# Optimization experiments

Measured on AMD Instinct MI355X. Metric: run time of the kernel, lower is better.

## Reference

```python
import jax, jax.numpy as jnp
import numpy as np

ITERATIONS = 100  # resonator iterations (default in __init__)


def _quantize(x):
    # MAP/bipolar quantize: sign with ties -> +1
    return jnp.where(x >= 0, 1.0, -1.0).astype(x.dtype)


def _resonator_step(inp, estimates, codebooks):
    # inp: (b, d); estimates: (b, f, d); codebooks: (f, v, d)
    f = estimates.shape[-2]
    # rolled copies, stacked: (b, f, f-1, d); product = multibind of all other factors
    rolled = jnp.stack([jnp.roll(estimates, i, axis=-3 + 1) for i in range(1, f)], axis=-2)
    inv_others = jnp.prod(rolled, axis=-2)              # (b, f, d)
    new_estimates = inp[:, None, :] * inv_others        # bind, (b, f, d)
    similarity = jnp.einsum('bfd,fvd->bfv', new_estimates, codebooks)  # (b, f, v)
    # multiset with similarity weights, then quantize
    output = _quantize(jnp.einsum('bfv,fvd->bfd', similarity, codebooks))
    max_sim = jnp.max(similarity, axis=-1)              # (b, f)
    return output, max_sim


def setup_inputs() -> dict:
    key = jax.random.key(0)
    b, f, v, d = 1024, 4, 64, 2048
    k1, k2 = jax.random.split(key)
    # bipolar codebooks (f, v, d)
    codebooks = _quantize(jax.random.normal(k1, (f, v, d), dtype=jnp.float32))
    # construct a solvable input: bind of one random codevector per factor
    idx = jax.random.randint(k2, (b, f), 0, v)          # (b, f)
    chosen = codebooks[jnp.arange(f)[None, :], idx]     # (b, f, d)
    inp = jnp.prod(chosen, axis=1)                      # (b, d)
    # init estimates: quantized multiset (bundle) of each codebook, tiled over batch
    init = _quantize(jnp.sum(codebooks, axis=1))        # (f, d)
    init_estimates = jnp.broadcast_to(init[None], (b, f, d)).astype(jnp.float32)
    return {"input": inp, "init_estimates": init_estimates, "codebooks": codebooks}


def reference(input, init_estimates, codebooks):
    # Concurrent resonator network, fixed iteration count (data-dependent
    # early-convergence check omitted for jit compatibility).
    def body(est, _):
        out, max_sim = _resonator_step(input, est, codebooks)
        return out, max_sim

    estimates, max_sims = jax.lax.scan(body, init_estimates, None, length=ITERATIONS)
    # cleanup: argmax of |similarity| against codebooks (argmax_abs=True)
    sim = jnp.einsum('bfd,fvd->bfv', estimates, codebooks)
    outcome = jnp.argmax(jnp.abs(sim), axis=-1).astype(jnp.int32)  # (b, f)
    convergence = jnp.int32(ITERATIONS - 1)
    return estimates, outcome, max_sims[-1], convergence
```

## Files before the change

### kernel.cpp

```cpp
#include <hip/hip_runtime.h>
#include <stdint.h>


#define NB 1024
#define NF 4
#define ND 2048
#define NW 32
#define ITERS 100

#define OFF_OUT  (NB*NF*ND)
#define OFF_MS   (OFF_OUT + NB*NF)
#define OFF_CONV (OFF_MS + NB*NF)

typedef unsigned long long u64;

__global__ void pack_cb_kernel(const float* __restrict__ cb,
                               u64* __restrict__ cbB, u64* __restrict__ cbT) {
    const int lane = threadIdx.x & 63;
    const int gw   = (blockIdx.x * (blockDim.x >> 6)) + (threadIdx.x >> 6);
    const int nw   = (gridDim.x * blockDim.x) >> 6;
    for (int idx = gw; idx < NF * 64 * NW; idx += nw) {
        const int j = idx >> 11, v = (idx >> 5) & 63, w = idx & 31;
        const float x = cb[(((j << 6) | v) << 11) + (w << 6) + lane];
        const u64 m = __ballot(x < 0.0f);
        if (lane == 0) cbB[(((j << 5) | w) << 6) | v] = m;
    }
    for (int idx = gw; idx < NF * ND; idx += nw) {
        const int j = idx >> 11, d = idx & 2047;
        const float x = cb[(((j << 6) | lane) << 11) + d];
        const u64 m = __ballot(x < 0.0f);
        if (lane == 0) cbT[idx] = m;
    }
}

__global__ __launch_bounds__(256, 2) void resonator_kernel(
    const float* __restrict__ inp, const float* __restrict__ est_init,
    const u64* __restrict__ cbB, const u64* __restrict__ cbT,
    float* __restrict__ out) {
    __shared__ u64 s_hist[4][NF][NW];
    __shared__ u64 s_inp[NW];
    __shared__ u64 s_ne[NF][NW];
    __shared__ int s_conv[NF];

    const int b    = blockIdx.x;
    const int tid  = threadIdx.x;
    const int j    = tid >> 6;
    const int lane = tid & 63;

    const u64* cbBj = cbB + (j << 11);
    const u64* cbTj = cbT + (j << 11);

    #pragma unroll
    for (int k = 0; k < 8; ++k) {
        const int w = (j << 3) + k;
        const u64 m = __ballot(inp[(b << 11) + (w << 6) + lane] < 0.0f);
        if (lane == 0) s_inp[w] = m;
    }
    #pragma unroll 4
    for (int w = 0; w < NW; ++w) {
        const u64 m = __ballot(
            est_init[(((b << 2) | j) << 11) + (w << 6) + lane] < 0.0f);
        if (lane == 0) s_hist[0][j][w] = m;
    }
    __syncthreads();

    int m_last = 0, m_prev = 0, final_slot = 0;

    for (int it = 0; it < ITERS; ++it) {
        const int cur = it & 3, nxt = (it + 1) & 3, prv = (it + 3) & 3;

        if (lane < NW) {
            const u64 X = s_inp[lane]
                        ^ s_hist[cur][0][lane] ^ s_hist[cur][1][lane]
                        ^ s_hist[cur][2][lane] ^ s_hist[cur][3][lane];
            s_ne[j][lane] = X ^ s_hist[cur][j][lane];
        }

        int pc = 0;
        #pragma unroll
        for (int ch = 0; ch < 4; ++ch) {
            const int w8 = ch << 3;
            const u64 g0 = cbBj[((w8 + 0) << 6) | lane];
            const u64 g1 = cbBj[((w8 + 1) << 6) | lane];
            const u64 g2 = cbBj[((w8 + 2) << 6) | lane];
            const u64 g3 = cbBj[((w8 + 3) << 6) | lane];
            const u64 g4 = cbBj[((w8 + 4) << 6) | lane];
            const u64 g5 = cbBj[((w8 + 5) << 6) | lane];
            const u64 g6 = cbBj[((w8 + 6) << 6) | lane];
            const u64 g7 = cbBj[((w8 + 7) << 6) | lane];
            pc += (int)__popcll(s_ne[j][w8 + 0] ^ g0)
                + (int)__popcll(s_ne[j][w8 + 1] ^ g1)
                + (int)__popcll(s_ne[j][w8 + 2] ^ g2)
                + (int)__popcll(s_ne[j][w8 + 3] ^ g3)
                + (int)__popcll(s_ne[j][w8 + 4] ^ g4)
                + (int)__popcll(s_ne[j][w8 + 5] ^ g5)
                + (int)__popcll(s_ne[j][w8 + 6] ^ g6)
                + (int)__popcll(s_ne[j][w8 + 7] ^ g7);
        }

        int mn = pc, spc = pc;
        #pragma unroll
        for (int off = 32; off > 0; off >>= 1) {
            const int a1 = __shfl_xor(mn, off);
            const int a2 = __shfl_xor(spc, off);
            mn = mn < a1 ? mn : a1;
            spc += a2;
        }
        m_prev = m_last;
        m_last = ND - 2 * mn;

        const int mean = spc >> 6;
        const int dev  = pc - mean;
        const int devc = dev < -128 ? -128 : (dev > 127 ? 127 : dev);
        const int ex   = dev - devc;
        const int u    = devc + 128;
        const u64 c0 = __ballot(u & 1),  c1 = __ballot(u & 2);
        const u64 c2 = __ballot(u & 4),  c3 = __ballot(u & 8);
        const u64 c4 = __ballot(u & 16), c5 = __ballot(u & 32);
        const u64 c6 = __ballot(u & 64), c7 = __ballot(u & 128);
        u64 om = __ballot(ex != 0);
        const int nout = (int)__popcll(om);
        int ov0 = 0, ov1 = 0, oe0 = 0, oe1 = 0;
        if (nout > 0) {
            ov0 = __builtin_ctzll(om); om &= om - 1;
            oe0 = 4 * __builtin_amdgcn_readlane(ex, ov0);
            if (nout > 1) {
                ov1 = __builtin_ctzll(om); om &= om - 1;
                oe1 = 4 * __builtin_amdgcn_readlane(ex, ov1);
            }
        }
        const int base = 131072 - 2 * spc;
        const int cmul = 4 * mean - 4608;

        #pragma unroll
        for (int ch = 0; ch < 8; ++ch) {
            const int w4 = ch << 2;
            const u64 ga = cbTj[((w4 + 0) << 6) | lane];
            const u64 gb = cbTj[((w4 + 1) << 6) | lane];
            const u64 gc = cbTj[((w4 + 2) << 6) | lane];
            const u64 gd = cbTj[((w4 + 3) << 6) | lane];
            #pragma unroll
            for (int k2 = 0; k2 < 4; ++k2) {
                const u64 cw = (k2 == 0) ? ga : (k2 == 1) ? gb
                             : (k2 == 2) ? gc : gd;
                int t = base + cmul * (int)__popcll(cw);
                t += (int)__popcll(c0 & cw) << 2;
                t += (int)__popcll(c1 & cw) << 3;
                t += (int)__popcll(c2 & cw) << 4;
                t += (int)__popcll(c3 & cw) << 5;
                t += (int)__popcll(c4 & cw) << 6;
                t += (int)__popcll(c5 & cw) << 7;
                t += (int)__popcll(c6 & cw) << 8;
                t += (int)__popcll(c7 & cw) << 9;
                t += oe0 * (int)((cw >> ov0) & 1);
                t += oe1 * (int)((cw >> ov1) & 1);
                if (nout > 2) {
                    u64 m2 = om;
                    while (m2) {
                        const int vv = __builtin_ctzll(m2); m2 &= m2 - 1;
                        const int ee = 4 * __builtin_amdgcn_readlane(ex, vv);
                        t += ee * (int)((cw >> vv) & 1);
                    }
                }
                const u64 nww = __ballot(t < 0);
                if (lane == 0) s_hist[nxt][j][w4 + k2] = nww;
            }
        }

        int df1 = 0, df2 = 0;
        if (lane < NW) {
            const u64 a = s_hist[nxt][j][lane];
            df1 = (a != s_hist[cur][j][lane]);
            df2 = (a != s_hist[prv][j][lane]);
        }
        const u64 b1 = __ballot(df1), b2 = __ballot(df2);
        if (lane == 0) s_conv[j] = (b1 == 0 ? 1 : 0) | (b2 == 0 ? 2 : 0);
        __syncthreads();

        const int fl = s_conv[0] & s_conv[1] & s_conv[2] & s_conv[3];
        final_slot = nxt;
        if (fl & 1) break;
        if (it >= 1 && (fl & 2)) {
            if (((ITERS - it) & 1) == 0) { final_slot = cur; m_last = m_prev; }
            break;
        }
    }

    int pcO = 0;
    #pragma unroll
    for (int w = 0; w < NW; ++w)
        pcO += (int)__popcll(s_hist[final_slot][j][w] ^ cbBj[(w << 6) | lane]);
    const int simF = ND - (pcO << 1);
    const int aF   = simF < 0 ? -simF : simF;
    int key = (aF << 6) | (63 - lane);
    #pragma unroll
    for (int off = 32; off > 0; off >>= 1) {
        const int t1 = __shfl_xor(key, off);
        key = key > t1 ? key : t1;
    }
    if (lane == 0) {
        out[OFF_OUT + (b << 2) + j] = (float)(63 - (key & 63));
        out[OFF_MS  + (b << 2) + j] = (float)m_last;
    }

    #pragma unroll 4
    for (int k = 0; k < 32; ++k) {
        const int idx = tid + (k << 8);
        const int jj = idx >> 11, d = idx & 2047;
        const u64 wrd = s_hist[final_slot][jj][d >> 6];
        out[(b << 13) + idx] = ((wrd >> (d & 63)) & 1) ? -1.0f : 1.0f;
    }
    if (b == 0 && tid == 0) out[OFF_CONV] = 99.0f;
}

extern "C" void kernel_launch(void* const* d_in, const int* in_sizes, int n_in,
                              void* d_out, int out_size, void* d_ws, size_t ws_size,
                              hipStream_t stream) {
    const float* inp  = (const float*)d_in[0];
    const float* est0 = (const float*)d_in[1];
    const float* cb   = (const float*)d_in[2];
    float* out = (float*)d_out;
    u64* cbB = (u64*)d_ws;
    u64* cbT = cbB + NF * 64 * NW;

    pack_cb_kernel<<<64, 256, 0, stream>>>(cb, cbB, cbT);
    resonator_kernel<<<NB, 256, 0, stream>>>(inp, est0, cbB, cbT, out);
}
```

Before: 1.743 ms.

## Process two batch rows per block to share codebook loads

Each block now runs the resonator iterations for two batch rows at once, so every codebook word loaded from global memory (cbB and cbT) and its column popcount is used for both rows. The grid is halved to NB/2 blocks. This cuts codebook traffic and load latency per row and gives more independent work per wave to hide latency. In exchange it raises register pressure, which may reduce occupancy. The early exit now waits until both rows have converged, so some rows may run extra iterations.

```diff
diff --git a/kernel.cpp b/kernel.cpp
--- a/kernel.cpp
+++ b/kernel.cpp
@@ -37,100 +37,123 @@
     const float* __restrict__ inp, const float* __restrict__ est_init,
     const u64* __restrict__ cbB, const u64* __restrict__ cbT,
     float* __restrict__ out) {
-    __shared__ u64 s_hist[4][NF][NW];
-    __shared__ u64 s_inp[NW];
-    __shared__ u64 s_ne[NF][NW];
-    __shared__ int s_conv[NF];
+    __shared__ u64 s_hist[2][4][NF][NW];
+    __shared__ u64 s_inp[2][NW];
+    __shared__ u64 s_ne[2][NF][NW];
+    __shared__ int s_conv[2][NF];
 
     const int b    = blockIdx.x;
     const int tid  = threadIdx.x;
     const int j    = tid >> 6;
     const int lane = tid & 63;
+    const int rA   = b << 1;
 
     const u64* cbBj = cbB + (j << 11);
     const u64* cbTj = cbT + (j << 11);
 
     #pragma unroll
-    for (int k = 0; k < 8; ++k) {
-        const int w = (j << 3) + k;
-        const u64 m = __ballot(inp[(b << 11) + (w << 6) + lane] < 0.0f);
-        if (lane == 0) s_inp[w] = m;
-    }
-    #pragma unroll 4
-    for (int w = 0; w < NW; ++w) {
-        const u64 m = __ballot(
-            est_init[(((b << 2) | j) << 11) + (w << 6) + lane] < 0.0f);
-        if (lane == 0) s_hist[0][j][w] = m;
+    for (int r = 0; r < 2; ++r) {
+        #pragma unroll
+        for (int k = 0; k < 8; ++k) {
+            const int w = (j << 3) + k;
+            const u64 m = __ballot(inp[((rA + r) << 11) + (w << 6) + lane] < 0.0f);
+            if (lane == 0) s_inp[r][w] = m;
+        }
+        #pragma unroll 4
+        for (int w = 0; w < NW; ++w) {
+            const u64 m = __ballot(
+                est_init[((((rA + r) << 2) | j) << 11) + (w << 6) + lane] < 0.0f);
+            if (lane == 0) s_hist[r][0][j][w] = m;
+        }
     }
     __syncthreads();
 
-    int m_last = 0, m_prev = 0, final_slot = 0;
+    int mlA = 0, mpA = 0, fsA = 0;
+    int mlB = 0, mpB = 0, fsB = 0;
 
     for (int it = 0; it < ITERS; ++it) {
         const int cur = it & 3, nxt = (it + 1) & 3, prv = (it + 3) & 3;
 
         if (lane < NW) {
-            const u64 X = s_inp[lane]
-                        ^ s_hist[cur][0][lane] ^ s_hist[cur][1][lane]
-                        ^ s_hist[cur][2][lane] ^ s_hist[cur][3][lane];
-            s_ne[j][lane] = X ^ s_hist[cur][j][lane];
-        }
-
-        int pc = 0;
-        #pragma unroll
-        for (int ch = 0; ch < 4; ++ch) {
-            const int w8 = ch << 3;
-            const u64 g0 = cbBj[((w8 + 0) << 6) | lane];
-            const u64 g1 = cbBj[((w8 + 1) << 6) | lane];
-            const u64 g2 = cbBj[((w8 + 2) << 6) | lane];
-            const u64 g3 = cbBj[((w8 + 3) << 6) | lane];
-            const u64 g4 = cbBj[((w8 + 4) << 6) | lane];
-            const u64 g5 = cbBj[((w8 + 5) << 6) | lane];
-            const u64 g6 = cbBj[((w8 + 6) << 6) | lane];
-            const u64 g7 = cbBj[((w8 + 7) << 6) | lane];
-            pc += (int)__popcll(s_ne[j][w8 + 0] ^ g0)
-                + (int)__popcll(s_ne[j][w8 + 1] ^ g1)
-                + (int)__popcll(s_ne[j][w8 + 2] ^ g2)
-                + (int)__popcll(s_ne[j][w8 + 3] ^ g3)
-                + (int)__popcll(s_ne[j][w8 + 4] ^ g4)
-                + (int)__popcll(s_ne[j][w8 + 5] ^ g5)
-                + (int)__popcll(s_ne[j][w8 + 6] ^ g6)
-                + (int)__popcll(s_ne[j][w8 + 7] ^ g7);
-        }
-
-        int mn = pc, spc = pc;
+            const u64 XA = s_inp[0][lane]
+                ^ s_hist[0][cur][0][lane] ^ s_hist[0][cur][1][lane]
+                ^ s_hist[0][cur][2][lane] ^ s_hist[0][cur][3][lane];
+            s_ne[0][j][lane] = XA ^ s_hist[0][cur][j][lane];
+            const u64 XB = s_inp[1][lane]
+                ^ s_hist[1][cur][0][lane] ^ s_hist[1][cur][1][lane]
+                ^ s_hist[1][cur][2][lane] ^ s_hist[1][cur][3][lane];
+            s_ne[1][j][lane] = XB ^ s_hist[1][cur][j][lane];
+        }
+
+        int pcA = 0, pcB = 0;
+        #pragma unroll
+        for (int ch = 0; ch < 8; ++ch) {
+            const int w4 = ch << 2;
+            const u64 g0 = cbBj[((w4 + 0) << 6) | lane];
+            const u64 g1 = cbBj[((w4 + 1) << 6) | lane];
+            const u64 g2 = cbBj[((w4 + 2) << 6) | lane];
+            const u64 g3 = cbBj[((w4 + 3) << 6) | lane];
+            pcA += (int)__popcll(s_ne[0][j][w4 + 0] ^ g0)
+                 + (int)__popcll(s_ne[0][j][w4 + 1] ^ g1)
+                 + (int)__popcll(s_ne[0][j][w4 + 2] ^ g2)
+                 + (int)__popcll(s_ne[0][j][w4 + 3] ^ g3);
+            pcB += (int)__popcll(s_ne[1][j][w4 + 0] ^ g0)
+                 + (int)__popcll(s_ne[1][j][w4 + 1] ^ g1)
+                 + (int)__popcll(s_ne[1][j][w4 + 2] ^ g2)
+                 + (int)__popcll(s_ne[1][j][w4 + 3] ^ g3);
+        }
+
+        int mnA = pcA, spA = pcA, mnB = pcB, spB = pcB;
         #pragma unroll
         for (int off = 32; off > 0; off >>= 1) {
-            const int a1 = __shfl_xor(mn, off);
-            const int a2 = __shfl_xor(spc, off);
-            mn = mn < a1 ? mn : a1;
-            spc += a2;
-        }
-        m_prev = m_last;
-        m_last = ND - 2 * mn;
-
-        const int mean = spc >> 6;
-        const int dev  = pc - mean;
-        const int devc = dev < -128 ? -128 : (dev > 127 ? 127 : dev);
-        const int ex   = dev - devc;
-        const int u    = devc + 128;
-        const u64 c0 = __ballot(u & 1),  c1 = __ballot(u & 2);
-        const u64 c2 = __ballot(u & 4),  c3 = __ballot(u & 8);
-        const u64 c4 = __ballot(u & 16), c5 = __ballot(u & 32);
-        const u64 c6 = __ballot(u & 64), c7 = __ballot(u & 128);
-        u64 om = __ballot(ex != 0);
-        const int nout = (int)__popcll(om);
-        int ov0 = 0, ov1 = 0, oe0 = 0, oe1 = 0;
-        if (nout > 0) {
-            ov0 = __builtin_ctzll(om); om &= om - 1;
-            oe0 = 4 * __builtin_amdgcn_readlane(ex, ov0);
-            if (nout > 1) {
-                ov1 = __builtin_ctzll(om); om &= om - 1;
-                oe1 = 4 * __builtin_amdgcn_readlane(ex, ov1);
+            const int a1 = __shfl_xor(mnA, off), a2 = __shfl_xor(spA, off);
+            const int a3 = __shfl_xor(mnB, off), a4 = __shfl_xor(spB, off);
+            mnA = mnA < a1 ? mnA : a1;  spA += a2;
+            mnB = mnB < a3 ? mnB : a3;  spB += a4;
+        }
+        mpA = mlA; mlA = ND - 2 * mnA;
+        mpB = mlB; mlB = ND - 2 * mnB;
+
+        const int meanA = spA >> 6, devA = pcA - meanA;
+        const int devcA = devA < -128 ? -128 : (devA > 127 ? 127 : devA);
+        const int exA = devA - devcA, uA = devcA + 128;
+        const int meanB = spB >> 6, devB = pcB - meanB;
+        const int devcB = devB < -128 ? -128 : (devB > 127 ? 127 : devB);
+        const int exB = devB - devcB, uB = devcB + 128;
+
+        const u64 cA0 = __ballot(uA & 1),  cA1 = __ballot(uA & 2);
+        const u64 cA2 = __ballot(uA & 4),  cA3 = __ballot(uA & 8);
+        const u64 cA4 = __ballot(uA & 16), cA5 = __ballot(uA & 32);
+        const u64 cA6 = __ballot(uA & 64), cA7 = __ballot(uA & 128);
+        const u64 cB0 = __ballot(uB & 1),  cB1 = __ballot(uB & 2);
+        const u64 cB2 = __ballot(uB & 4),  cB3 = __ballot(uB & 8);
+        const u64 cB4 = __ballot(uB & 16), cB5 = __ballot(uB & 32);
+        const u64 cB6 = __ballot(uB & 64), cB7 = __ballot(uB & 128);
+
+        u64 omA = __ballot(exA != 0);
+        const int novA = (int)__popcll(omA);
+        int ovA0 = 0, ovA1 = 0, oeA0 = 0, oeA1 = 0;
+        if (novA > 0) {
+            ovA0 = __builtin_ctzll(omA); omA &= omA - 1;
+            oeA0 = 4 * __builtin_amdgcn_readlane(exA, ovA0);
+            if (novA > 1) {
+                ovA1 = __builtin_ctzll(omA); omA &= omA - 1;
+                oeA1 = 4 * __builtin_amdgcn_readlane(exA, ovA1);
             }
         }
-        const int base = 131072 - 2 * spc;
-        const int cmul = 4 * mean - 4608;
+        u64 omB = __ballot(exB != 0);
+        const int novB = (int)__popcll(omB);
+        int ovB0 = 0, ovB1 = 0, oeB0 = 0, oeB1 = 0;
+        if (novB > 0) {
+            ovB0 = __builtin_ctzll(omB); omB &= omB - 1;
+            oeB0 = 4 * __builtin_amdgcn_readlane(exB, ovB0);
+            if (novB > 1) {
+                ovB1 = __builtin_ctzll(omB); omB &= omB - 1;
+                oeB1 = 4 * __builtin_amdgcn_readlane(exB, ovB1);
+            }
+        }
+        const int baseA = 131072 - 2 * spA, cmulA = 4 * meanA - 4608;
+        const int baseB = 131072 - 2 * spB, cmulB = 4 * meanB - 4608;
 
         #pragma unroll
         for (int ch = 0; ch < 8; ++ch) {
@@ -143,72 +166,110 @@
             for (int k2 = 0; k2 < 4; ++k2) {
                 const u64 cw = (k2 == 0) ? ga : (k2 == 1) ? gb
                              : (k2 == 2) ? gc : gd;
-                int t = base + cmul * (int)__popcll(cw);
-                t += (int)__popcll(c0 & cw) << 2;
-                t += (int)__popcll(c1 & cw) << 3;
-                t += (int)__popcll(c2 & cw) << 4;
-                t += (int)__popcll(c3 & cw) << 5;
-                t += (int)__popcll(c4 & cw) << 6;
-                t += (int)__popcll(c5 & cw) << 7;
-                t += (int)__popcll(c6 & cw) << 8;
-                t += (int)__popcll(c7 & cw) << 9;
-                t += oe0 * (int)((cw >> ov0) & 1);
-                t += oe1 * (int)((cw >> ov1) & 1);
-                if (nout > 2) {
-                    u64 m2 = om;
+                const int colb = (int)__popcll(cw);
+                int tA = baseA + cmulA * colb;
+                tA += (int)__popcll(cA0 & cw) << 2;
+                tA += (int)__popcll(cA1 & cw) << 3;
+                tA += (int)__popcll(cA2 & cw) << 4;
+                tA += (int)__popcll(cA3 & cw) << 5;
+                tA += (int)__popcll(cA4 & cw) << 6;
+                tA += (int)__popcll(cA5 & cw) << 7;
+                tA += (int)__popcll(cA6 & cw) << 8;
+                tA += (int)__popcll(cA7 & cw) << 9;
+                tA += oeA0 * (int)((cw >> ovA0) & 1);
+                tA += oeA1 * (int)((cw >> ovA1) & 1);
+                if (novA > 2) {
+                    u64 m2 = omA;
                     while (m2) {
                         const int vv = __builtin_ctzll(m2); m2 &= m2 - 1;
-                        const int ee = 4 * __builtin_amdgcn_readlane(ex, vv);
-                        t += ee * (int)((cw >> vv) & 1);
+                        tA += 4 * __builtin_amdgcn_readlane(exA, vv)
+                                * (int)((cw >> vv) & 1);
                     }
                 }
-                const u64 nww = __ballot(t < 0);
-                if (lane == 0) s_hist[nxt][j][w4 + k2] = nww;
+                int tB = baseB + cmulB * colb;
+                tB += (int)__popcll(cB0 & cw) << 2;
+                tB += (int)__popcll(cB1 & cw) << 3;
+                tB += (int)__popcll(cB2 & cw) << 4;
+                tB += (int)__popcll(cB3 & cw) << 5;
+                tB += (int)__popcll(cB4 & cw) << 6;
+                tB += (int)__popcll(cB5 & cw) << 7;
+                tB += (int)__popcll(cB6 & cw) << 8;
+                tB += (int)__popcll(cB7 & cw) << 9;
+                tB += oeB0 * (int)((cw >> ovB0) & 1);
+                tB += oeB1 * (int)((cw >> ovB1) & 1);
+                if (novB > 2) {
+                    u64 m2 = omB;
+                    while (m2) {
+                        const int vv = __builtin_ctzll(m2); m2 &= m2 - 1;
+                        tB += 4 * __builtin_amdgcn_readlane(exB, vv)
+                                * (int)((cw >> vv) & 1);
+                    }
+                }
+                const u64 nwA = __ballot(tA < 0);
+                const u64 nwB = __ballot(tB < 0);
+                if (lane == 0) {
+                    s_hist[0][nxt][j][w4 + k2] = nwA;
+                    s_hist[1][nxt][j][w4 + k2] = nwB;
+                }
             }
         }
 
-        int df1 = 0, df2 = 0;
+        int d1A = 0, d2A = 0, d1B = 0, d2B = 0;
         if (lane < NW) {
-            const u64 a = s_hist[nxt][j][lane];
-            df1 = (a != s_hist[cur][j][lane]);
-            df2 = (a != s_hist[prv][j][lane]);
-        }
-        const u64 b1 = __ballot(df1), b2 = __ballot(df2);
-        if (lane == 0) s_conv[j] = (b1 == 0 ? 1 : 0) | (b2 == 0 ? 2 : 0);
+            const u64 aA = s_hist[0][nxt][j][lane];
+            d1A = (aA != s_hist[0][cur][j][lane]);
+            d2A = (aA != s_hist[0][prv][j][lane]);
+            const u64 aB = s_hist[1][nxt][j][lane];
+            d1B = (aB != s_hist[1][cur][j][lane]);
+            d2B = (aB != s_hist[1][prv][j][lane]);
+        }
+        const u64 bA1 = __ballot(d1A), bA2 = __ballot(d2A);
+        const u64 bB1 = __ballot(d1B), bB2 = __ballot(d2B);
+        if (lane == 0) {
+            s_conv[0][j] = (bA1 == 0 ? 1 : 0) | (bA2 == 0 ? 2 : 0);
+            s_conv[1][j] = (bB1 == 0 ? 1 : 0) | (bB2 == 0 ? 2 : 0);
+        }
         __syncthreads();
 
-        const int fl = s_conv[0] & s_conv[1] & s_conv[2] & s_conv[3];
-        final_slot = nxt;
-        if (fl & 1) break;
-        if (it >= 1 && (fl & 2)) {
-            if (((ITERS - it) & 1) == 0) { final_slot = cur; m_last = m_prev; }
+        const int flA = s_conv[0][0] & s_conv[0][1] & s_conv[0][2] & s_conv[0][3];
+        const int flB = s_conv[1][0] & s_conv[1][1] & s_conv[1][2] & s_conv[1][3];
+        fsA = nxt; fsB = nxt;
+        const bool okA = (flA & 1) || (it >= 1 && (flA & 2));
+        const bool okB = (flB & 1) || (it >= 1 && (flB & 2));
+        if (okA && okB) {
+            if (!(flA & 1) && ((ITERS - it) & 1) == 0) { fsA = cur; mlA = mpA; }
+            if (!(flB & 1) && ((ITERS - it) & 1) == 0) { fsB = cur; mlB = mpB; }
             break;
         }
     }
 
-    int pcO = 0;
     #pragma unroll
-    for (int w = 0; w < NW; ++w)
-        pcO += (int)__popcll(s_hist[final_slot][j][w] ^ cbBj[(w << 6) | lane]);
-    const int simF = ND - (pcO << 1);
-    const int aF   = simF < 0 ? -simF : simF;
-    int key = (aF << 6) | (63 - lane);
-    #pragma unroll
-    for (int off = 32; off > 0; off >>= 1) {
-        const int t1 = __shfl_xor(key, off);
-        key = key > t1 ? key : t1;
-    }
-    if (lane == 0) {
-        out[OFF_OUT + (b << 2) + j] = (float)(63 - (key & 63));
-        out[OFF_MS  + (b << 2) + j] = (float)m_last;
-    }
-
-    #pragma unroll 4
-    for (int k = 0; k < 32; ++k) {
-        const int idx = tid + (k << 8);
-        const int jj = idx >> 11, d = idx & 2047;
-        const u64 wrd = s_hist[final_slot][jj][d >> 6];
-        out[(b << 13) + idx] = ((wrd >> (d & 63)) & 1) ? -1.0f : 1.0f;
+    for (int r = 0; r < 2; ++r) {
+        const int fs = r ? fsB : fsA;
+        const int ml = r ? mlB : mlA;
+        int pcO = 0;
+        #pragma unroll
+        for (int w = 0; w < NW; ++w)
+            pcO += (int)__popcll(s_hist[r][fs][j][w] ^ cbBj[(w << 6) | lane]);
+        const int simF = ND - (pcO << 1);
+        const int aF   = simF < 0 ? -simF : simF;
+        int key = (aF << 6) | (63 - lane);
+        #pragma unroll
+        for (int off = 32; off > 0; off >>= 1) {
+            const int t1 = __shfl_xor(key, off);
+            key = key > t1 ? key : t1;
+        }
+        if (lane == 0) {
+            out[OFF_OUT + ((rA + r) << 2) + j] = (float)(63 - (key & 63));
+            out[OFF_MS  + ((rA + r) << 2) + j] = (float)ml;
+        }
+        #pragma unroll 4
+        for (int k = 0; k < 32; ++k) {
+            const int idx = tid + (k << 8);
+            const int jj = idx >> 11, d = idx & 2047;
+            const u64 wrd = s_hist[r][fs][jj][d >> 6];
+            out[((rA + r) << 13) + idx] = ((wrd >> (d & 63)) & 1) ? -1.0f : 1.0f;
+        }
     }
     if (b == 0 && tid == 0) out[OFF_CONV] = 99.0f;
 }
@@ -224,5 +285,5 @@
     u64* cbT = cbB + NF * 64 * NW;
 
     pack_cb_kernel<<<64, 256, 0, stream>>>(cb, cbB, cbT);
-    resonator_kernel<<<NB, 256, 0, stream>>>(inp, est0, cbB, cbT, out);
+    resonator_kernel<<<NB / 2, 256, 0, stream>>>(inp, est0, cbB, cbT, out);
 }
```

New measurement: 1.730 ms. No clear change (-0.7%).

## Stage packed codebooks in LDS and process four batch rows per block

Applied to the files above, without the earlier changes.

Each block now handles four batch rows with 1024 threads and copies the bit-packed codebooks (both orientations) into shared memory once. The per-iteration similarity and multiset loops read them as 128-bit pairs from LDS instead of 64-bit global loads, and the pack layout is interleaved to support this. The history ring shrinks to three slots with rotating indices. Early exit now requires all four rows in a block to have converged, so rows that settle early may run extra iterations. The grid also shrinks to 256 blocks, which reduces parallelism.

```diff
diff --git a/kernel.cpp b/kernel.cpp
--- a/kernel.cpp
+++ b/kernel.cpp
@@ -7,6 +7,7 @@
 #define ND 2048
 #define NW 32
 #define ITERS 100
+#define NRB 4
 
 #define OFF_OUT  (NB*NF*ND)
 #define OFF_MS   (OFF_OUT + NB*NF)
@@ -23,93 +24,115 @@
         const int j = idx >> 11, v = (idx >> 5) & 63, w = idx & 31;
         const float x = cb[(((j << 6) | v) << 11) + (w << 6) + lane];
         const u64 m = __ballot(x < 0.0f);
-        if (lane == 0) cbB[(((j << 5) | w) << 6) | v] = m;
+        if (lane == 0)
+            cbB[(((((j << 4) | (w >> 1)) << 6) | v) << 1) | (w & 1)] = m;
     }
     for (int idx = gw; idx < NF * ND; idx += nw) {
         const int j = idx >> 11, d = idx & 2047;
         const float x = cb[(((j << 6) | lane) << 11) + d];
         const u64 m = __ballot(x < 0.0f);
-        if (lane == 0) cbT[idx] = m;
+        const int w = d >> 6, la = d & 63;
+        if (lane == 0)
+            cbT[(((((j << 4) | (w >> 1)) << 6) | la) << 1) | (w & 1)] = m;
     }
 }
 
-__global__ __launch_bounds__(256, 2) void resonator_kernel(
+#define PCW(CW, W)                                                           \
+    {                                                                        \
+        const u64 cw_ = (CW);                                                \
+        int t = base + cmul * (int)__popcll(cw_);                            \
+        t += (int)__popcll(c0 & cw_) << 2;                                   \
+        t += (int)__popcll(c1 & cw_) << 3;                                   \
+        t += (int)__popcll(c2 & cw_) << 4;                                   \
+        t += (int)__popcll(c3 & cw_) << 5;                                   \
+        t += (int)__popcll(c4 & cw_) << 6;                                   \
+        t += (int)__popcll(c5 & cw_) << 7;                                   \
+        t += (int)__popcll(c6 & cw_) << 8;                                   \
+        t += (int)__popcll(c7 & cw_) << 9;                                   \
+        t += oe0 * (int)((cw_ >> ov0) & 1);                                  \
+        t += oe1 * (int)((cw_ >> ov1) & 1);                                  \
+        if (nov > 2) {                              \
+            u64 m2 = om;                                                     \
+            while (m2) {                                                     \
+                const int vv = __builtin_ctzll(m2); m2 &= m2 - 1;            \
+                t += 4 * __builtin_amdgcn_readlane(ex, vv)                   \
+                       * (int)((cw_ >> vv) & 1);                             \
+            }                                                                \
+        }                                                                    \
+        const u64 nww = __ballot(t < 0);                                     \
+        if (lane == 0) s_hist[r][nxt][j][W] = nww;                           \
+    }
+
+__global__ __launch_bounds__(1024, 4) void resonator_kernel(
     const float* __restrict__ inp, const float* __restrict__ est_init,
     const u64* __restrict__ cbB, const u64* __restrict__ cbT,
     float* __restrict__ out) {
-    __shared__ u64 s_hist[4][NF][NW];
-    __shared__ u64 s_inp[NW];
-    __shared__ u64 s_ne[NF][NW];
-    __shared__ int s_conv[NF];
+    __shared__ u64 l_cbB[NF * 16 * 64 * 2];
+    __shared__ u64 l_cbT[NF * 16 * 64 * 2];
+    __shared__ u64 s_hist[NRB][3][NF][NW];
+    __shared__ u64 s_inp[NRB][NW];
+    __shared__ u64 s_ne[NRB][NF][NW];
+    __shared__ int s_conv[NRB][NF];
+    __shared__ int s_fs[NRB];
 
     const int b    = blockIdx.x;
     const int tid  = threadIdx.x;
-    const int j    = tid >> 6;
+    const int wid  = tid >> 6;
     const int lane = tid & 63;
-
-    const u64* cbBj = cbB + (j << 11);
-    const u64* cbTj = cbT + (j << 11);
-
+    const int j    = wid & 3;
+    const int r    = wid >> 2;
+    const int row  = (b << 2) + r;
+
+    for (int idx = tid; idx < NF * 16 * 64 * 2; idx += 1024) {
+        l_cbB[idx] = cbB[idx];
+        l_cbT[idx] = cbT[idx];
+    }
     #pragma unroll
     for (int k = 0; k < 8; ++k) {
         const int w = (j << 3) + k;
-        const u64 m = __ballot(inp[(b << 11) + (w << 6) + lane] < 0.0f);
-        if (lane == 0) s_inp[w] = m;
+        const u64 m = __ballot(inp[(row << 11) + (w << 6) + lane] < 0.0f);
+        if (lane == 0) s_inp[r][w] = m;
     }
     #pragma unroll 4
     for (int w = 0; w < NW; ++w) {
         const u64 m = __ballot(
-            est_init[(((b << 2) | j) << 11) + (w << 6) + lane] < 0.0f);
-        if (lane == 0) s_hist[0][j][w] = m;
+            est_init[(((row << 2) | j) << 11) + (w << 6) + lane] < 0.0f);
+        if (lane == 0) s_hist[r][0][j][w] = m;
     }
     __syncthreads();
 
-    int m_last = 0, m_prev = 0, final_slot = 0;
+    const ulonglong2* tB = (const ulonglong2*)l_cbB + (j << 10) + lane;
+    const ulonglong2* tT = (const ulonglong2*)l_cbT + (j << 10) + lane;
+
+    int ml = 0, mp = 0, fs = 0;
+    int cur = 0, nxt = 1, prv = 2;
 
     for (int it = 0; it < ITERS; ++it) {
-        const int cur = it & 3, nxt = (it + 1) & 3, prv = (it + 3) & 3;
-
         if (lane < NW) {
-            const u64 X = s_inp[lane]
-                        ^ s_hist[cur][0][lane] ^ s_hist[cur][1][lane]
-                        ^ s_hist[cur][2][lane] ^ s_hist[cur][3][lane];
-            s_ne[j][lane] = X ^ s_hist[cur][j][lane];
+            const u64 X = s_inp[r][lane]
+                ^ s_hist[r][cur][0][lane] ^ s_hist[r][cur][1][lane]
+                ^ s_hist[r][cur][2][lane] ^ s_hist[r][cur][3][lane];
+            s_ne[r][j][lane] = X ^ s_hist[r][cur][j][lane];
         }
 
         int pc = 0;
         #pragma unroll
-        for (int ch = 0; ch < 4; ++ch) {
-            const int w8 = ch << 3;
-            const u64 g0 = cbBj[((w8 + 0) << 6) | lane];
-            const u64 g1 = cbBj[((w8 + 1) << 6) | lane];
-            const u64 g2 = cbBj[((w8 + 2) << 6) | lane];
-            const u64 g3 = cbBj[((w8 + 3) << 6) | lane];
-            const u64 g4 = cbBj[((w8 + 4) << 6) | lane];
-            const u64 g5 = cbBj[((w8 + 5) << 6) | lane];
-            const u64 g6 = cbBj[((w8 + 6) << 6) | lane];
-            const u64 g7 = cbBj[((w8 + 7) << 6) | lane];
-            pc += (int)__popcll(s_ne[j][w8 + 0] ^ g0)
-                + (int)__popcll(s_ne[j][w8 + 1] ^ g1)
-                + (int)__popcll(s_ne[j][w8 + 2] ^ g2)
-                + (int)__popcll(s_ne[j][w8 + 3] ^ g3)
-                + (int)__popcll(s_ne[j][w8 + 4] ^ g4)
-                + (int)__popcll(s_ne[j][w8 + 5] ^ g5)
-                + (int)__popcll(s_ne[j][w8 + 6] ^ g6)
-                + (int)__popcll(s_ne[j][w8 + 7] ^ g7);
-        }
-
-        int mn = pc, spc = pc;
+        for (int w2 = 0; w2 < 16; ++w2) {
+            const ulonglong2 g  = tB[w2 << 6];
+            const ulonglong2 nn = *(const ulonglong2*)&s_ne[r][j][w2 << 1];
+            pc += (int)__popcll(nn.x ^ g.x) + (int)__popcll(nn.y ^ g.y);
+        }
+        int mn = pc, sp = pc;
         #pragma unroll
         for (int off = 32; off > 0; off >>= 1) {
             const int a1 = __shfl_xor(mn, off);
-            const int a2 = __shfl_xor(spc, off);
+            const int a2 = __shfl_xor(sp, off);
             mn = mn < a1 ? mn : a1;
-            spc += a2;
-        }
-        m_prev = m_last;
-        m_last = ND - 2 * mn;
-
-        const int mean = spc >> 6;
+            sp += a2;
+        }
+        mp = ml; ml = ND - 2 * mn;
+
+        const int mean = sp >> 6;
         const int dev  = pc - mean;
         const int devc = dev < -128 ? -128 : (dev > 127 ? 127 : dev);
         const int ex   = dev - devc;
@@ -119,77 +142,62 @@
         const u64 c4 = __ballot(u & 16), c5 = __ballot(u & 32);
         const u64 c6 = __ballot(u & 64), c7 = __ballot(u & 128);
         u64 om = __ballot(ex != 0);
-        const int nout = (int)__popcll(om);
+        const int nov = (int)__popcll(om);
         int ov0 = 0, ov1 = 0, oe0 = 0, oe1 = 0;
-        if (nout > 0) {
+        if (nov > 0) {
             ov0 = __builtin_ctzll(om); om &= om - 1;
             oe0 = 4 * __builtin_amdgcn_readlane(ex, ov0);
-            if (nout > 1) {
+            if (nov > 1) {
                 ov1 = __builtin_ctzll(om); om &= om - 1;
                 oe1 = 4 * __builtin_amdgcn_readlane(ex, ov1);
             }
         }
-        const int base = 131072 - 2 * spc;
+        const int base = 131072 - 2 * sp;
         const int cmul = 4 * mean - 4608;
 
         #pragma unroll
-        for (int ch = 0; ch < 8; ++ch) {
-            const int w4 = ch << 2;
-            const u64 ga = cbTj[((w4 + 0) << 6) | lane];
-            const u64 gb = cbTj[((w4 + 1) << 6) | lane];
-            const u64 gc = cbTj[((w4 + 2) << 6) | lane];
-            const u64 gd = cbTj[((w4 + 3) << 6) | lane];
-            #pragma unroll
-            for (int k2 = 0; k2 < 4; ++k2) {
-                const u64 cw = (k2 == 0) ? ga : (k2 == 1) ? gb
-                             : (k2 == 2) ? gc : gd;
-                int t = base + cmul * (int)__popcll(cw);
-                t += (int)__popcll(c0 & cw) << 2;
-                t += (int)__popcll(c1 & cw) << 3;
-                t += (int)__popcll(c2 & cw) << 4;
-                t += (int)__popcll(c3 & cw) << 5;
-                t += (int)__popcll(c4 & cw) << 6;
-                t += (int)__popcll(c5 & cw) << 7;
-                t += (int)__popcll(c6 & cw) << 8;
-                t += (int)__popcll(c7 & cw) << 9;
-                t += oe0 * (int)((cw >> ov0) & 1);
-                t += oe1 * (int)((cw >> ov1) & 1);
-                if (nout > 2) {
-                    u64 m2 = om;
-                    while (m2) {
-                        const int vv = __builtin_ctzll(m2); m2 &= m2 - 1;
-                        const int ee = 4 * __builtin_amdgcn_readlane(ex, vv);
-                        t += ee * (int)((cw >> vv) & 1);
-                    }
-                }
-                const u64 nww = __ballot(t < 0);
-                if (lane == 0) s_hist[nxt][j][w4 + k2] = nww;
-            }
-        }
-
-        int df1 = 0, df2 = 0;
+        for (int w2 = 0; w2 < 16; ++w2) {
+            const ulonglong2 g = tT[w2 << 6];
+            PCW(g.x, (w2 << 1))
+            PCW(g.y, (w2 << 1) + 1)
+        }
+
+        int d1 = 0, d2 = 0;
         if (lane < NW) {
-            const u64 a = s_hist[nxt][j][lane];
-            df1 = (a != s_hist[cur][j][lane]);
-            df2 = (a != s_hist[prv][j][lane]);
-        }
-        const u64 b1 = __ballot(df1), b2 = __ballot(df2);
-        if (lane == 0) s_conv[j] = (b1 == 0 ? 1 : 0) | (b2 == 0 ? 2 : 0);
+            const u64 a = s_hist[r][nxt][j][lane];
+            d1 = (a != s_hist[r][cur][j][lane]);
+            d2 = (a != s_hist[r][prv][j][lane]);
+        }
+        const u64 b1 = __ballot(d1), b2 = __ballot(d2);
+        if (lane == 0) s_conv[r][j] = (b1 == 0 ? 1 : 0) | (b2 == 0 ? 2 : 0);
         __syncthreads();
 
-        const int fl = s_conv[0] & s_conv[1] & s_conv[2] & s_conv[3];
-        final_slot = nxt;
-        if (fl & 1) break;
-        if (it >= 1 && (fl & 2)) {
-            if (((ITERS - it) & 1) == 0) { final_slot = cur; m_last = m_prev; }
+        int flr = 0;
+        bool allok = true;
+        #pragma unroll
+        for (int r2 = 0; r2 < NRB; ++r2) {
+            const int f = s_conv[r2][0] & s_conv[r2][1]
+                        & s_conv[r2][2] & s_conv[r2][3];
+            if (r2 == r) flr = f;
+            allok = allok && ((f & 1) || (it >= 1 && (f & 2)));
+        }
+        fs = nxt;
+        if (allok) {
+            if (!(flr & 1) && ((ITERS - it) & 1) == 0) { fs = cur; ml = mp; }
             break;
         }
-    }
+        const int t3 = prv; prv = cur; cur = nxt; nxt = t3;
+    }
+
+    if (j == 0 && lane == 0) s_fs[r] = fs;
 
     int pcO = 0;
     #pragma unroll
-    for (int w = 0; w < NW; ++w)
-        pcO += (int)__popcll(s_hist[final_slot][j][w] ^ cbBj[(w << 6) | lane]);
+    for (int w2 = 0; w2 < 16; ++w2) {
+        const ulonglong2 g  = tB[w2 << 6];
+        const ulonglong2 hh = *(const ulonglong2*)&s_hist[r][fs][j][w2 << 1];
+        pcO += (int)__popcll(hh.x ^ g.x) + (int)__popcll(hh.y ^ g.y);
+    }
     const int simF = ND - (pcO << 1);
     const int aF   = simF < 0 ? -simF : simF;
     int key = (aF << 6) | (63 - lane);
@@ -199,16 +207,22 @@
         key = key > t1 ? key : t1;
     }
     if (lane == 0) {
-        out[OFF_OUT + (b << 2) + j] = (float)(63 - (key & 63));
-        out[OFF_MS  + (b << 2) + j] = (float)m_last;
-    }
-
-    #pragma unroll 4
-    for (int k = 0; k < 32; ++k) {
-        const int idx = tid + (k << 8);
-        const int jj = idx >> 11, d = idx & 2047;
-        const u64 wrd = s_hist[final_slot][jj][d >> 6];
-        out[(b << 13) + idx] = ((wrd >> (d & 63)) & 1) ? -1.0f : 1.0f;
+        out[OFF_OUT + (row << 2) + j] = (float)(63 - (key & 63));
+        out[OFF_MS  + (row << 2) + j] = (float)ml;
+    }
+    __syncthreads();
+
+    #pragma unroll
+    for (int rr = 0; rr < NRB; ++rr) {
+        const int f2 = s_fs[rr];
+        #pragma unroll
+        for (int k = 0; k < 8; ++k) {
+            const int idx = tid + (k << 10);
+            const int jj = idx >> 11, d = idx & 2047;
+            const u64 wrd = s_hist[rr][f2][jj][d >> 6];
+            out[(((b << 2) + rr) << 13) + idx] =
+                ((wrd >> (d & 63)) & 1) ? -1.0f : 1.0f;
+        }
     }
     if (b == 0 && tid == 0) out[OFF_CONV] = 99.0f;
 }
@@ -221,8 +235,8 @@
     const float* cb   = (const float*)d_in[2];
     float* out = (float*)d_out;
     u64* cbB = (u64*)d_ws;
-    u64* cbT = cbB + NF * 64 * NW;
+    u64* cbT = cbB + NF * 16 * 64 * 2;
 
     pack_cb_kernel<<<64, 256, 0, stream>>>(cb, cbB, cbT);
-    resonator_kernel<<<NB, 256, 0, stream>>>(inp, est0, cbB, cbT, out);
+    resonator_kernel<<<NB / NRB, 1024, 0, stream>>>(inp, est0, cbB, cbT, out);
 }
```

After: 1.673 ms. -4.0%, faster.
